# Kernel optimization log

Hardware: AMD Instinct MI355X
Metric: run time of the kernel (lower is better)

Reference implementation:

```python
import jax, jax.numpy as jnp
from jax import lax
import numpy as np

B, T = 256, 512
CHAR_SIZE, CHAR_DIM, HIDDEN = 10000, 50, 256
HALF = HIDDEN // 2  # per-direction hidden size


def _lstm_dir(x, Wih, Whh, bih, bhh, reverse):
    # x: [B,T,D]; Wih: [4H,D]; Whh: [4H,H]; gate order i,f,g,o (PyTorch)
    Bsz = x.shape[0]
    H = Whh.shape[1]
    xg = jnp.einsum('btd,gd->btg', x, Wih) + bih + bhh  # precompute input gates [B,T,4H]
    def step(carry, gt):
        h, c = carry
        g = gt + h @ Whh.T
        i, f, gg, o = jnp.split(g, 4, axis=-1)
        c = jax.nn.sigmoid(f) * c + jax.nn.sigmoid(i) * jnp.tanh(gg)
        h = jax.nn.sigmoid(o) * jnp.tanh(c)
        return (h, c), h
    init = (jnp.zeros((Bsz, H), x.dtype), jnp.zeros((Bsz, H), x.dtype))
    _, hs = lax.scan(step, init, jnp.swapaxes(xg, 0, 1), reverse=reverse)
    return jnp.swapaxes(hs, 0, 1)  # [B,T,H]


def setup_inputs() -> dict:
    key = jax.random.key(0)
    ks = jax.random.split(key, 10)
    scale = np.sqrt(3.0 / CHAR_DIM)
    inp = {
        'user_text_idx': jax.random.randint(ks[0], (B, T), 0, CHAR_SIZE),
        'masks': jnp.ones((B, T), jnp.float32),
        'emb': jax.random.uniform(ks[1], (CHAR_SIZE, CHAR_DIM), jnp.float32, -scale, scale),
        'Wih_f': jax.random.normal(ks[2], (4 * HALF, CHAR_DIM), jnp.float32) * 0.08,
        'Whh_f': jax.random.normal(ks[3], (4 * HALF, HALF), jnp.float32) * 0.08,
        'bih_f': jnp.zeros((4 * HALF,), jnp.float32),
        'bhh_f': jnp.zeros((4 * HALF,), jnp.float32),
        'Wih_b': jax.random.normal(ks[4], (4 * HALF, CHAR_DIM), jnp.float32) * 0.08,
        'Whh_b': jax.random.normal(ks[5], (4 * HALF, HALF), jnp.float32) * 0.08,
        'bih_b': jnp.zeros((4 * HALF,), jnp.float32),
        'bhh_b': jnp.zeros((4 * HALF,), jnp.float32),
    }
    return inp


def reference(user_text_idx, masks, emb, Wih_f, Whh_f, bih_f, bhh_f, Wih_b, Whh_b, bih_b, bhh_b):
    x = emb[user_text_idx]                                  # [B,T,D] embedding lookup
    h_f = _lstm_dir(x, Wih_f, Whh_f, bih_f, bhh_f, False)   # forward direction
    h_b = _lstm_dir(x, Wih_b, Whh_b, bih_b, bhh_b, True)    # backward direction
    out = jnp.concatenate([h_f, h_b], axis=-1)              # [B,T,HIDDEN]
    out = out - (1.0 - masks[..., None]) * 1e8              # mask pad positions
    return jnp.max(out, axis=-2)                            # masked max-pool -> [B,HIDDEN]
```

## Files before the change

### kernel.cpp

```cpp
#include <hip/hip_runtime.h>
#include <hip/hip_fp16.h>


#define TT 512
#define CH 2

typedef _Float16 f16;
typedef _Float16 f16x8 __attribute__((ext_vector_type(8)));
typedef float f32x4 __attribute__((ext_vector_type(4)));
typedef unsigned int u32;
typedef unsigned short u16;

static __device__ __forceinline__ u32 packh2(float lo, float hi) {
    union { struct { f16 x, y; } h; u32 u; } cv;
    cv.h.x = (f16)lo; cv.h.y = (f16)hi;
    return cv.u;
}
static __device__ __forceinline__ u16 f16bits(float v) {
    union { f16 h; u16 u; } cv; cv.h = (f16)v; return cv.u;
}
static __device__ __forceinline__ float fexp(float x) {
    return __builtin_amdgcn_exp2f(x * 1.44269504088896341f);
}
static __device__ __forceinline__ float frcp(float x) {
    return __builtin_amdgcn_rcpf(x);
}
static __device__ __forceinline__ float sigf(float x) {
    return frcp(1.f + fexp(-x));
}
static __device__ __forceinline__ float swz8(float x) {
    union { float f; int i; } c; c.f = x;
    c.i = __builtin_amdgcn_ds_swizzle(c.i, 0x201F);
    return c.f;
}
static __device__ __forceinline__ float sel4(f32x4 v, int q) {
    return (q & 2) ? ((q & 1) ? v[3] : v[2]) : ((q & 1) ? v[1] : v[0]);
}

__global__ __attribute__((amdgpu_flat_work_group_size(512, 512),
                          amdgpu_waves_per_eu(2, 2)))
void bilstm_mfma_ch2_kernel(const int* __restrict__ idx,
                            const float* __restrict__ masks,
                            const float* __restrict__ emb,
                            const float* __restrict__ Wih_f, const float* __restrict__ Whh_f,
                            const float* __restrict__ bih_f, const float* __restrict__ bhh_f,
                            const float* __restrict__ Wih_b, const float* __restrict__ Whh_b,
                            const float* __restrict__ bih_b, const float* __restrict__ bhh_b,
                            float* __restrict__ out)
{
    __shared__ __align__(16) unsigned char Hbuf[2][6 * 1024];
    __shared__ u16 idx16[CH * TT];
    __shared__ u32 mbits[TT];

    const int tid  = threadIdx.x;
    const int lane = tid & 63;
    const int wv   = tid >> 6;
    const int l15  = lane & 15;
    const int c4   = lane >> 4;
    const int d    = blockIdx.x & 1;
    const int g    = blockIdx.x >> 1;
    const int b0   = g * CH;
    const int rev  = d;

    const int chain = l15 & 1;
    const int cp    = l15 >> 1;
    const int flag  = cp >> 2;
    const int q     = cp & 3;

    const float* Wih = d ? Wih_b : Wih_f;
    const float* Whh = d ? Whh_b : Whh_f;
    const float* bih = d ? bih_b : bih_f;
    const float* bhh = d ? bhh_b : bhh_f;

    for (int i = tid; i < CH * TT; i += 512) {
        const int m = i >> 9, t = i & 511;
        idx16[i] = (u16)idx[(b0 + m) * TT + t];
    }
    if (tid < TT) {
        u32 mb = 0;
        for (int m = 0; m < CH; ++m)
            mb |= (masks[(b0 + m) * TT + tid] != 0.f ? 1u : 0u) << m;
        mbits[tid] = mb;
    }
    for (int i = tid; i < 2 * 6 * 1024 / 4; i += 512)
        ((u32*)Hbuf)[i] = 0u;

    f16x8 w[6][4];
#pragma unroll
    for (int gt = 0; gt < 4; ++gt) {
        const int n = (wv + gt * 8) * 16 + l15;
#pragma unroll
        for (int jj = 0; jj < 4; ++jj) {
            const float2 e = *(const float2*)(Wih + n * 50 + c4 * 8 + jj * 2);
            w[0][gt][2 * jj]     = (f16)e.x;
            w[0][gt][2 * jj + 1] = (f16)e.y;
        }
#pragma unroll
        for (int j = 0; j < 8; ++j) {
            const int k = 32 + c4 * 8 + j;
            float v = 0.f;
            if (k < 50) v = Wih[n * 50 + k];
            w[1][gt][j] = (f16)v;
        }
#pragma unroll
        for (int kt = 2; kt < 6; ++kt) {
            const int kh = (kt - 2) * 32 + c4 * 8;
            const float4 e0 = *(const float4*)(Whh + n * 128 + kh);
            const float4 e1 = *(const float4*)(Whh + n * 128 + kh + 4);
            w[kt][gt][0] = (f16)e0.x; w[kt][gt][1] = (f16)e0.y;
            w[kt][gt][2] = (f16)e0.z; w[kt][gt][3] = (f16)e0.w;
            w[kt][gt][4] = (f16)e1.x; w[kt][gt][5] = (f16)e1.y;
            w[kt][gt][6] = (f16)e1.z; w[kt][gt][7] = (f16)e1.w;
        }
    }

    const int hd  = wv * 16 + c4 * 4 + q;
    const float b_i = bih[hd]       + bhh[hd];
    const float b_f = bih[128 + hd] + bhh[128 + hd];
    const float b_g = bih[256 + hd] + bhh[256 + hd];
    const float b_o = bih[384 + hd] + bhh[384 + hd];

    __syncthreads();

    if (tid < 400) {
        const int pm = tid / 25, ps = tid % 25;
        const int t0  = rev ? (TT - 1) : 0;
        const int row = idx16[(pm & 1) * TT + t0];
        const float2 e = *(const float2*)(emb + row * 50 + ps * 2);
        const int k0 = 2 * ps;
        const int kt = k0 >> 5, c4k = (k0 >> 3) & 3, j = k0 & 7;
        *(u32*)(&Hbuf[0][(kt << 10) + ((c4k * 16 + pm) << 4) + (j << 1)]) =
            packh2(e.x, e.y);
    }
    __syncthreads();

    float cst0 = 0.f, rm0 = -3e38f;

    const int k0h    = 64 + hd;
    const int wb_kt  = k0h >> 5;
    const int wb_c4k = (k0h >> 3) & 3;
    const int wb_j   = k0h & 7;
    const int wb_off = (wb_kt << 10) + ((wb_c4k * 16 + chain) << 4) + (wb_j << 1)
                     + flag * 128;

    for (int s = 0; s < TT; ++s) {
        const int cur = s & 1;
        const int t   = rev ? (TT - 1 - s) : s;

        float2 e;
        int pk0 = 0;
        const bool pf = (tid < 400) && (s + 1 < TT);
        const int pm = tid / 25, ps = tid % 25;
        if (pf) {
            const int t1  = rev ? (TT - 2 - s) : (s + 1);
            const int row = idx16[(pm & 1) * TT + t1];
            e = *(const float2*)(emb + row * 50 + ps * 2);
            pk0 = 2 * ps;
        }

        const unsigned char* hb = &Hbuf[cur][0];
        const f32x4 z = {0.f, 0.f, 0.f, 0.f};
        f32x4 ai = z, af = z, ag = z, ao = z;
#pragma unroll
        for (int kt = 0; kt < 6; ++kt) {
            const f16x8 bf = *(const f16x8*)(hb + (kt << 10) + (lane << 4));
            ai = __builtin_amdgcn_mfma_f32_16x16x32_f16(w[kt][0], bf, ai, 0, 0, 0);
            af = __builtin_amdgcn_mfma_f32_16x16x32_f16(w[kt][1], bf, af, 0, 0, 0);
            ag = __builtin_amdgcn_mfma_f32_16x16x32_f16(w[kt][2], bf, ag, 0, 0, 0);
            ao = __builtin_amdgcn_mfma_f32_16x16x32_f16(w[kt][3], bf, ao, 0, 0, 0);
        }

        const float iv = sel4(ai, q) + b_i;
        const float fv = sel4(af, q) + b_f;
        const float gv = sel4(ag, q) + b_g;
        const float ov = sel4(ao, q) + b_o;

        const bool fB = (flag != 0);
        const float u = fB ? (gv + gv) : fv;
        const float v = fB ? ov : iv;
        const float su = sigf(u);
        const float sv = sigf(v);
        const float tg_send = 2.f * su - 1.f;
        const float tgx = swz8(tg_send);
        const float svx = swz8(sv);
        const float cc = su * cst0 + sv * tgx;
        cst0 = cc;
        const float ccx = swz8(cc);
        const float cc_use = fB ? ccx : cc;
        const float th = 2.f * sigf(cc_use + cc_use) - 1.f;
        const float so_use = fB ? sv : svx;
        const float hh = so_use * th;

        const float pen = ((mbits[t] >> chain) & 1u) ? 0.f : 1e8f;
        rm0 = fmaxf(rm0, hh - pen);

        unsigned char* nb = &Hbuf[cur ^ 1][0];
        {
            const u16 pk = f16bits(hh);
            *(u16*)(nb + wb_off)      = pk;
            *(u16*)(nb + wb_off + 32) = pk;
            *(u16*)(nb + wb_off + 64) = pk;
            *(u16*)(nb + wb_off + 96) = pk;
        }
        if (pf) {
            const int kt = pk0 >> 5, c4k = (pk0 >> 3) & 3, j = pk0 & 7;
            *(u32*)(nb + (kt << 10) + ((c4k * 16 + pm) << 4) + (j << 1)) =
                packh2(e.x, e.y);
        }
        __syncthreads();
    }

    if (!flag) {
        out[(b0 + chain) * 256 + d * 128 + hd] = rm0;
    }
}

extern "C" void kernel_launch(void* const* d_in, const int* in_sizes, int n_in,
                              void* d_out, int out_size, void* d_ws, size_t ws_size,
                              hipStream_t stream) {
    const int*   idx   = (const int*)d_in[0];
    const float* masks = (const float*)d_in[1];
    const float* emb   = (const float*)d_in[2];
    const float* Wih_f = (const float*)d_in[3];
    const float* Whh_f = (const float*)d_in[4];
    const float* bih_f = (const float*)d_in[5];
    const float* bhh_f = (const float*)d_in[6];
    const float* Wih_b = (const float*)d_in[7];
    const float* Whh_b = (const float*)d_in[8];
    const float* bih_b = (const float*)d_in[9];
    const float* bhh_b = (const float*)d_in[10];
    float* out = (float*)d_out;

    bilstm_mfma_ch2_kernel<<<dim3(256), dim3(512), 0, stream>>>(
        idx, masks, emb,
        Wih_f, Whh_f, bih_f, bhh_f,
        Wih_b, Whh_b, bih_b, bhh_b,
        out);
}
```

Measured before the change: 424.6 us.

## Process one sequence per block and swap swizzles for DPP lane exchanges

The kernel now handles one batch row per block instead of two, doubling the grid so two blocks can share a CU, and raises waves-per-EU to 4. The goal is to hide the latency of the serial recurrence by interleaving independent blocks. Cross-lane exchanges move from ds_swizzle to DPP moves, and the hidden-state writeback packs neighbouring values into two 32-bit LDS stores instead of four 16-bit ones. The cost is doubled total MFMA and embedding-fetch work, and a tighter register budget that could cause spills with 96 VGPRs of resident weights.

```diff
diff --git a/kernel.cpp b/kernel.cpp
--- a/kernel.cpp
+++ b/kernel.cpp
@@ -3,7 +3,6 @@
 
 
 #define TT 512
-#define CH 2
 
 typedef _Float16 f16;
 typedef _Float16 f16x8 __attribute__((ext_vector_type(8)));
@@ -16,9 +15,6 @@
     cv.h.x = (f16)lo; cv.h.y = (f16)hi;
     return cv.u;
 }
-static __device__ __forceinline__ u16 f16bits(float v) {
-    union { f16 h; u16 u; } cv; cv.h = (f16)v; return cv.u;
-}
 static __device__ __forceinline__ float fexp(float x) {
     return __builtin_amdgcn_exp2f(x * 1.44269504088896341f);
 }
@@ -28,9 +24,14 @@
 static __device__ __forceinline__ float sigf(float x) {
     return frcp(1.f + fexp(-x));
 }
-static __device__ __forceinline__ float swz8(float x) {
+static __device__ __forceinline__ float xor8(float x) {
     union { float f; int i; } c; c.f = x;
-    c.i = __builtin_amdgcn_ds_swizzle(c.i, 0x201F);
+    c.i = __builtin_amdgcn_mov_dpp(c.i, 0x128, 0xF, 0xF, false);
+    return c.f;
+}
+static __device__ __forceinline__ float xor1(float x) {
+    union { float f; int i; } c; c.f = x;
+    c.i = __builtin_amdgcn_mov_dpp(c.i, 0xB1, 0xF, 0xF, false);
     return c.f;
 }
 static __device__ __forceinline__ float sel4(f32x4 v, int q) {
@@ -38,8 +39,8 @@
 }
 
 __global__ __attribute__((amdgpu_flat_work_group_size(512, 512),
-                          amdgpu_waves_per_eu(2, 2)))
-void bilstm_mfma_ch2_kernel(const int* __restrict__ idx,
+                          amdgpu_waves_per_eu(4, 4)))
+void bilstm_mfma_ch1_kernel(const int* __restrict__ idx,
                             const float* __restrict__ masks,
                             const float* __restrict__ emb,
                             const float* __restrict__ Wih_f, const float* __restrict__ Whh_f,
@@ -49,7 +50,7 @@
                             float* __restrict__ out)
 {
     __shared__ __align__(16) unsigned char Hbuf[2][6 * 1024];
-    __shared__ u16 idx16[CH * TT];
+    __shared__ u16 idx16[TT];
     __shared__ u32 mbits[TT];
 
     const int tid  = threadIdx.x;
@@ -58,29 +59,20 @@
     const int l15  = lane & 15;
     const int c4   = lane >> 4;
     const int d    = blockIdx.x & 1;
-    const int g    = blockIdx.x >> 1;
-    const int b0   = g * CH;
+    const int b0   = blockIdx.x >> 1;
     const int rev  = d;
 
-    const int chain = l15 & 1;
-    const int cp    = l15 >> 1;
-    const int flag  = cp >> 2;
-    const int q     = cp & 3;
+    const int q    = l15 & 3;
+    const bool fB  = (l15 >> 3) != 0;
 
     const float* Wih = d ? Wih_b : Wih_f;
     const float* Whh = d ? Whh_b : Whh_f;
     const float* bih = d ? bih_b : bih_f;
     const float* bhh = d ? bhh_b : bhh_f;
 
-    for (int i = tid; i < CH * TT; i += 512) {
-        const int m = i >> 9, t = i & 511;
-        idx16[i] = (u16)idx[(b0 + m) * TT + t];
-    }
     if (tid < TT) {
-        u32 mb = 0;
-        for (int m = 0; m < CH; ++m)
-            mb |= (masks[(b0 + m) * TT + tid] != 0.f ? 1u : 0u) << m;
-        mbits[tid] = mb;
+        idx16[tid] = (u16)idx[b0 * TT + tid];
+        mbits[tid] = (masks[b0 * TT + tid] != 0.f) ? 1u : 0u;
     }
     for (int i = tid; i < 2 * 6 * 1024 / 4; i += 512)
         ((u32*)Hbuf)[i] = 0u;
@@ -125,7 +117,7 @@
     if (tid < 400) {
         const int pm = tid / 25, ps = tid % 25;
         const int t0  = rev ? (TT - 1) : 0;
-        const int row = idx16[(pm & 1) * TT + t0];
+        const int row = idx16[t0];
         const float2 e = *(const float2*)(emb + row * 50 + ps * 2);
         const int k0 = 2 * ps;
         const int kt = k0 >> 5, c4k = (k0 >> 3) & 3, j = k0 & 7;
@@ -136,12 +128,13 @@
 
     float cst0 = 0.f, rm0 = -3e38f;
 
-    const int k0h    = 64 + hd;
+    const int hdp    = hd & ~1;
+    const int k0h    = 64 + hdp;
     const int wb_kt  = k0h >> 5;
     const int wb_c4k = (k0h >> 3) & 3;
     const int wb_j   = k0h & 7;
-    const int wb_off = (wb_kt << 10) + ((wb_c4k * 16 + chain) << 4) + (wb_j << 1)
-                     + flag * 128;
+    const int uu     = ((l15 >> 2) << 1) | (l15 & 1);
+    const int wb_off = (wb_kt << 10) + ((wb_c4k * 16 + 2 * uu) << 4) + (wb_j << 1);
 
     for (int s = 0; s < TT; ++s) {
         const int cur = s & 1;
@@ -153,7 +146,7 @@
         const int pm = tid / 25, ps = tid % 25;
         if (pf) {
             const int t1  = rev ? (TT - 2 - s) : (s + 1);
-            const int row = idx16[(pm & 1) * TT + t1];
+            const int row = idx16[t1];
             e = *(const float2*)(emb + row * 50 + ps * 2);
             pk0 = 2 * ps;
         }
@@ -175,32 +168,30 @@
         const float gv = sel4(ag, q) + b_g;
         const float ov = sel4(ao, q) + b_o;
 
-        const bool fB = (flag != 0);
-        const float u = fB ? (gv + gv) : fv;
-        const float v = fB ? ov : iv;
-        const float su = sigf(u);
-        const float sv = sigf(v);
+        const float u_in = fB ? (gv + gv) : fv;
+        const float v_in = fB ? ov : iv;
+        const float su = sigf(u_in);
+        const float sv = sigf(v_in);
         const float tg_send = 2.f * su - 1.f;
-        const float tgx = swz8(tg_send);
-        const float svx = swz8(sv);
+        const float tgx = xor8(tg_send);
+        const float svx = xor8(sv);
         const float cc = su * cst0 + sv * tgx;
         cst0 = cc;
-        const float ccx = swz8(cc);
+        const float ccx = xor8(cc);
         const float cc_use = fB ? ccx : cc;
         const float th = 2.f * sigf(cc_use + cc_use) - 1.f;
         const float so_use = fB ? sv : svx;
         const float hh = so_use * th;
 
-        const float pen = ((mbits[t] >> chain) & 1u) ? 0.f : 1e8f;
+        const float pen = (mbits[t] & 1u) ? 0.f : 1e8f;
         rm0 = fmaxf(rm0, hh - pen);
 
         unsigned char* nb = &Hbuf[cur ^ 1][0];
         {
-            const u16 pk = f16bits(hh);
-            *(u16*)(nb + wb_off)      = pk;
-            *(u16*)(nb + wb_off + 32) = pk;
-            *(u16*)(nb + wb_off + 64) = pk;
-            *(u16*)(nb + wb_off + 96) = pk;
+            const float hx = xor1(hh);
+            const u32 pk = (q & 1) ? packh2(hx, hh) : packh2(hh, hx);
+            *(u32*)(nb + wb_off)      = pk;
+            *(u32*)(nb + wb_off + 16) = pk;
         }
         if (pf) {
             const int kt = pk0 >> 5, c4k = (pk0 >> 3) & 3, j = pk0 & 7;
@@ -210,8 +201,8 @@
         __syncthreads();
     }
 
-    if (!flag) {
-        out[(b0 + chain) * 256 + d * 128 + hd] = rm0;
+    if (l15 < 4) {
+        out[b0 * 256 + d * 128 + hd] = rm0;
     }
 }
 
@@ -231,7 +222,7 @@
     const float* bhh_b = (const float*)d_in[10];
     float* out = (float*)d_out;
 
-    bilstm_mfma_ch2_kernel<<<dim3(256), dim3(512), 0, stream>>>(
+    bilstm_mfma_ch1_kernel<<<dim3(512), dim3(512), 0, stream>>>(
         idx, masks, emb,
         Wih_f, Whh_f, bih_f, bhh_f,
         Wih_b, Whh_b, bih_b, bhh_b,
```

Result: slower. 941.7 us (+121.8%).
